# Performance work log

Hardware: AMD Instinct MI355X
Metric: run time of the kernel (lower is better)

## Reference

```python
import jax, jax.numpy as jnp
import numpy as np

N_QUBITS = 12
ENTANGLER_REPS = 2  # qml.layer(BasicEntanglerLayers, reps=2): 2 rings of CNOTs


def _apply_rx(state, theta, q, n):
    # state: (B, 2^n) complex; theta: (B,) per-sample RX angle on wire q
    B = state.shape[0]
    st = state.reshape(B, 2 ** q, 2, -1)
    c = jnp.cos(theta * 0.5)[:, None, None]
    s = jnp.sin(theta * 0.5)[:, None, None]
    s0, s1 = st[:, :, 0, :], st[:, :, 1, :]
    new0 = c * s0 - 1j * s * s1
    new1 = -1j * s * s0 + c * s1
    return jnp.stack([new0, new1], axis=2).reshape(B, -1)


def _apply_cnot(state, c, t, n):
    # CNOT with control wire c, target wire t (wire 0 = most significant bit)
    B = state.shape[0]
    st = state.reshape((B,) + (2,) * n)
    a0 = jnp.take(st, jnp.array([0]), axis=c + 1)
    a1 = jnp.take(st, jnp.array([1]), axis=c + 1)
    a1 = jnp.flip(a1, axis=t + 1)  # flip target when control = 1
    return jnp.concatenate([a0, a1], axis=c + 1).reshape(B, -1)


def quantum_latent(z, q_params):
    # Batched statevector simulation of: RX(z_i + p_i) on each wire,
    # then ENTANGLER_REPS rings of CNOT(i, (i+1)%n), measure <Z_i> per wire.
    B, n = z.shape
    theta = z + q_params[None, :]
    state = jnp.zeros((B, 2 ** n), dtype=jnp.complex64).at[:, 0].set(1.0)
    for q in range(n):
        state = _apply_rx(state, theta[:, q], q, n)
    for _ in range(ENTANGLER_REPS):
        for q in range(n):
            state = _apply_cnot(state, q, (q + 1) % n, n)
    probs = jnp.real(state * jnp.conj(state))  # (B, 2^n)
    expz = []
    for q in range(n):
        p = probs.reshape(B, 2 ** q, 2, -1)
        expz.append(p[:, :, 0, :].sum(axis=(1, 2)) - p[:, :, 1, :].sum(axis=(1, 2)))
    return jnp.stack(expz, axis=1)  # (B, n) float32


def setup_inputs() -> dict:
    key = jax.random.key(0)
    ks = jax.random.split(key, 16)
    B, D, H1, H2, L = 2048, 4096, 2048, 1024, N_QUBITS

    def lin(k, i, o):
        return (jax.random.normal(k, (o, i), jnp.float32) / np.sqrt(i)).astype(jnp.float32)

    return {
        "x": jax.random.normal(ks[0], (B, D), jnp.float32),
        "enc_w1": lin(ks[1], D, H1), "enc_b1": jnp.zeros((H1,), jnp.float32),
        "enc_w2": lin(ks[2], H1, H2), "enc_b2": jnp.zeros((H2,), jnp.float32),
        "enc_w3": lin(ks[3], H2, L), "enc_b3": jnp.zeros((L,), jnp.float32),
        "q_params": 0.1 * jax.random.normal(ks[4], (L,), jnp.float32),
        "dec_w1": lin(ks[5], L, H2), "dec_b1": jnp.zeros((H2,), jnp.float32),
        "dec_w2": lin(ks[6], H2, H1), "dec_b2": jnp.zeros((H1,), jnp.float32),
        "dec_w3": lin(ks[7], H1, D), "dec_b3": jnp.zeros((D,), jnp.float32),
    }


def reference(x, enc_w1, enc_b1, enc_w2, enc_b2, enc_w3, enc_b3, q_params,
              dec_w1, dec_b1, dec_w2, dec_b2, dec_w3, dec_b3):
    # encoder: Linear+ReLU (dropout=0 -> identity), Linear+ReLU, Linear
    h = jax.nn.relu(x @ enc_w1.T + enc_b1)
    h = jax.nn.relu(h @ enc_w2.T + enc_b2)
    z = h @ enc_w3.T + enc_b3  # (B, latent_dim)
    qz = quantum_latent(z, q_params)  # (B, latent_dim)
    # decoder (reversed hidden dims)
    h = jax.nn.relu(qz @ dec_w1.T + dec_b1)
    h = jax.nn.relu(h @ dec_w2.T + dec_b2)
    recon = h @ dec_w3.T + dec_b3  # (B, input_dim)
    return recon
```

## Files before the change

kernel.cpp:

```cpp
#include <hip/hip_runtime.h>
#include <hip/hip_bf16.h>


typedef __bf16 bf16x8 __attribute__((ext_vector_type(8)));
typedef __bf16 bf16x4 __attribute__((ext_vector_type(4)));
typedef float  f32x4  __attribute__((ext_vector_type(4)));

__device__ __forceinline__ void async16(const void* g, void* l) {
    __builtin_amdgcn_global_load_lds(
        (const __attribute__((address_space(1))) unsigned int*)g,
        (__attribute__((address_space(3))) unsigned int*)l,
        16, 0, 0);
}

template<int VM> __device__ __forceinline__ void wait_vm_lgkm0() {
    if constexpr (VM == 0)      asm volatile("s_waitcnt vmcnt(0) lgkmcnt(0)" ::: "memory");
    else if constexpr (VM == 4) asm volatile("s_waitcnt vmcnt(4) lgkmcnt(0)" ::: "memory");
    else if constexpr (VM == 6) asm volatile("s_waitcnt vmcnt(6) lgkmcnt(0)" ::: "memory");
    else if constexpr (VM == 8) asm volatile("s_waitcnt vmcnt(8) lgkmcnt(0)" ::: "memory");
    else static_assert(VM == 0 || VM == 4 || VM == 6 || VM == 8, "unsupported VM");
}

template <int BM, int BN, typename TOUT, bool RELU>
__global__ __launch_bounds__(256) void gemm_pipe(
    const __bf16* __restrict__ A, const __bf16* __restrict__ W,
    const float* __restrict__ bias, TOUT* __restrict__ C,
    int M, int N, int K)
{
    constexpr int CHA = BM / 32, CHB = BN / 32, LLOADS = CHA + CHB;
    constexpr int ABYTES = BM * 128, BUFB = (BM + BN) * 128;
    constexpr int WMR = BM / 2, WNC = BN / 2;
    constexpr int NI = WMR / 16, NJ = WNC / 16;

    extern __shared__ char smem[];

    const int t    = threadIdx.x;
    const int lane = t & 63;
    const int w    = t >> 6;
    const int bm   = blockIdx.y * BM;
    const int bn   = blockIdx.x * BN;

    const int sr  = lane >> 3;
    const int scs = (lane & 7) ^ sr;
    const __bf16* gA = A + (size_t)(bm + w * 8 + sr) * K + scs * 8;
    const __bf16* gB = W + (size_t)(bn + w * 8 + sr) * K + scs * 8;

    const int lm = lane & 15;
    const int lh = lane >> 4;
    const int wm = w >> 1, wn = w & 1;
    const int axor = lm & 7;

    f32x4 acc[NI][NJ] = {};

    auto STAGE = [&](int buf, int tt) {
        char* la = smem + buf * BUFB + w * 1024;
        char* lb = smem + buf * BUFB + ABYTES + w * 1024;
        const __bf16* ga = gA + (size_t)tt * 64;
        const __bf16* gb = gB + (size_t)tt * 64;
        #pragma unroll
        for (int j = 0; j < CHA; ++j) async16(ga + (size_t)32 * K * j, la + j * 4096);
        #pragma unroll
        for (int j = 0; j < CHB; ++j) async16(gb + (size_t)32 * K * j, lb + j * 4096);
    };

    auto COMPUTE = [&](int buf) {
        char* base = smem + buf * BUFB;
        bf16x8 a[2][NI], b[2][NJ];
        #pragma unroll
        for (int kh = 0; kh < 2; ++kh) {
            #pragma unroll
            for (int i = 0; i < NI; ++i)
                a[kh][i] = *(const bf16x8*)(base + (wm * WMR + i * 16 + lm) * 128
                                            + ((kh * 4 + lh) ^ axor) * 16);
            #pragma unroll
            for (int j = 0; j < NJ; ++j)
                b[kh][j] = *(const bf16x8*)(base + ABYTES + (wn * WNC + j * 16 + lm) * 128
                                            + ((kh * 4 + lh) ^ axor) * 16);
        }
        __builtin_amdgcn_s_setprio(1);
        #pragma unroll
        for (int kh = 0; kh < 2; ++kh)
            #pragma unroll
            for (int i = 0; i < NI; ++i)
                #pragma unroll
                for (int j = 0; j < NJ; ++j)
                    acc[i][j] = __builtin_amdgcn_mfma_f32_16x16x32_bf16(
                        a[kh][i], b[kh][j], acc[i][j], 0, 0, 0);
        __builtin_amdgcn_s_setprio(0);
    };

    const int NT = K >> 6;
    STAGE(0, 0);
    STAGE(1, 1);

    for (int tt = 0; tt < NT; ++tt) {
        if (tt < NT - 1) wait_vm_lgkm0<LLOADS>();
        else             wait_vm_lgkm0<0>();
        __builtin_amdgcn_s_barrier();
        __builtin_amdgcn_sched_barrier(0);
        COMPUTE(tt & 1);
        if (tt + 2 < NT) {
            asm volatile("s_waitcnt lgkmcnt(0)" ::: "memory");
            __builtin_amdgcn_s_barrier();
            __builtin_amdgcn_sched_barrier(0);
            STAGE(tt & 1, tt + 2);
        }
    }

    #pragma unroll
    for (int i = 0; i < NI; ++i) {
        const int row0 = bm + wm * WMR + i * 16 + lh * 4;
        #pragma unroll
        for (int j = 0; j < NJ; ++j) {
            const int col = bn + wn * WNC + j * 16 + lm;
            const float bv = bias[col];
            #pragma unroll
            for (int r = 0; r < 4; ++r) {
                float v = acc[i][j][r] + bv;
                if (RELU) v = fmaxf(v, 0.f);
                C[(size_t)(row0 + r) * N + col] = (TOUT)v;
            }
        }
    }
}

__device__ __forceinline__ void cvt8(const float* __restrict__ src,
                                     __bf16* __restrict__ dst, int g) {
    const float4* p = reinterpret_cast<const float4*>(src) + (size_t)g * 2;
    float4 a = p[0], b = p[1];
    bf16x8 v;
    v[0] = (__bf16)a.x; v[1] = (__bf16)a.y; v[2] = (__bf16)a.z; v[3] = (__bf16)a.w;
    v[4] = (__bf16)b.x; v[5] = (__bf16)b.y; v[6] = (__bf16)b.z; v[7] = (__bf16)b.w;
    reinterpret_cast<bf16x8*>(dst)[g] = v;
}

__global__ __launch_bounds__(256) void cvt_pair(
    const float* __restrict__ s0, __bf16* __restrict__ d0, int n0,
    const float* __restrict__ s1, __bf16* __restrict__ d1)
{
    int i = blockIdx.x * 256 + threadIdx.x;
    if (i < n0) cvt8(s0, d0, i);
    else        cvt8(s1, d1, i - n0);
}

__global__ __launch_bounds__(256) void cvt_triple(
    const float* __restrict__ s0, __bf16* __restrict__ d0, int n0,
    const float* __restrict__ s1, __bf16* __restrict__ d1, int n1,
    const float* __restrict__ s2, __bf16* __restrict__ d2)
{
    int i = blockIdx.x * 256 + threadIdx.x;
    if (i < n0)           cvt8(s0, d0, i);
    else if (i < n0 + n1) cvt8(s1, d1, i - n0);
    else                  cvt8(s2, d2, i - n0 - n1);
}

__constant__ unsigned short kSMask[12] = {
    0xAAB, 0xFFD, 0xFFA, 0xFF5, 0xFEA, 0xFD5,
    0xFAA, 0xF55, 0xEAA, 0xD55, 0xAAA, 0x555
};

__global__ __launch_bounds__(256) void enc3q_dec1(
    const float* __restrict__ H2,
    const float* __restrict__ W3,
    const float* __restrict__ b3,
    const float* __restrict__ qp,
    const float* __restrict__ dW1,
    const float* __restrict__ db1,
    __bf16* __restrict__ H3)
{
    const int b    = blockIdx.x;
    const int t    = threadIdx.x;
    const int lane = t & 63;
    const int wid  = t >> 6;

    float h[4];
    #pragma unroll
    for (int i = 0; i < 4; ++i) h[i] = H2[(size_t)b * 1024 + t + i * 256];

    __shared__ float wred[4][12];
    __shared__ float ctheta[12];
    __shared__ float qz[12];

    #pragma unroll 1
    for (int n = 0; n < 12; ++n) {
        float p = 0.f;
        #pragma unroll
        for (int i = 0; i < 4; ++i)
            p = fmaf(h[i], W3[n * 1024 + t + i * 256], p);
        #pragma unroll
        for (int off = 32; off > 0; off >>= 1)
            p += __shfl_down(p, off);
        if (lane == 0) wred[wid][n] = p;
    }
    __syncthreads();

    if (t < 12) {
        float z = wred[0][t] + wred[1][t] + wred[2][t] + wred[3][t]
                + b3[t] + qp[t];
        ctheta[t] = cosf(z);
    }
    __syncthreads();

    if (t < 12) {
        const unsigned m = kSMask[t];
        float prod = 1.f;
        #pragma unroll
        for (int j = 0; j < 12; ++j)
            if ((m >> j) & 1) prod *= ctheta[j];
        qz[t] = prod;
    }
    __syncthreads();

    bf16x4 v;
    #pragma unroll
    for (int j = 0; j < 4; ++j) {
        const int n = t * 4 + j;
        float acc = db1[n];
        #pragma unroll
        for (int k = 0; k < 12; ++k)
            acc = fmaf(qz[k], dW1[n * 12 + k], acc);
        v[j] = (__bf16)fmaxf(acc, 0.f);
    }
    *reinterpret_cast<bf16x4*>(&H3[(size_t)b * 1024 + t * 4]) = v;
}

extern "C" void kernel_launch(void* const* d_in, const int* in_sizes, int n_in,
                              void* d_out, int out_size, void* d_ws, size_t ws_size,
                              hipStream_t stream) {
    const float* x   = (const float*)d_in[0];
    const float* w1  = (const float*)d_in[1];
    const float* b1  = (const float*)d_in[2];
    const float* w2  = (const float*)d_in[3];
    const float* b2  = (const float*)d_in[4];
    const float* w3  = (const float*)d_in[5];
    const float* b3  = (const float*)d_in[6];
    const float* qp  = (const float*)d_in[7];
    const float* dw1 = (const float*)d_in[8];
    const float* db1 = (const float*)d_in[9];
    const float* dw2 = (const float*)d_in[10];
    const float* db2 = (const float*)d_in[11];
    const float* dw3 = (const float*)d_in[12];
    const float* db3 = (const float*)d_in[13];
    float* out = (float*)d_out;

    const int B = 2048, D = 4096, H1 = 2048, H2 = 1024;

    char* ws = (char*)d_ws;
    __bf16* xb   = (__bf16*)(ws);
    __bf16* dw3b = (__bf16*)(ws);
    __bf16* w1b  = (__bf16*)(ws + 16777216);
    float*  h2f  = (float*) (ws + 16777216);
    __bf16* w2b  = (__bf16*)(ws + 25165824);
    __bf16* h3b  = (__bf16*)(ws + 25165824);
    __bf16* dw2b = (__bf16*)(ws + 29360128);
    __bf16* h1b  = (__bf16*)(ws + 33554432);
    __bf16* h4b  = (__bf16*)(ws + 33554432);

    dim3 blk(256);

    cvt_pair<<<dim3(8192), blk, 0, stream>>>(x, xb, 1048576, w1, w1b);

    gemm_pipe<128, 64, __bf16, true><<<dim3(H1 / 64, B / 128), blk, 49152, stream>>>(
        xb, w1b, b1, h1b, B, H1, D);

    cvt_triple<<<dim3(6144), blk, 0, stream>>>(w2, w2b, 262144,
                                               dw2, dw2b, 262144,
                                               dw3, dw3b);

    gemm_pipe<64, 64, float, true><<<dim3(H2 / 64, B / 64), blk, 32768, stream>>>(
        h1b, w2b, b2, h2f, B, H2, H1);

    enc3q_dec1<<<dim3(B), blk, 0, stream>>>(h2f, w3, b3, qp, dw1, db1, h3b);

    gemm_pipe<128, 64, __bf16, true><<<dim3(H1 / 64, B / 128), blk, 49152, stream>>>(
        h3b, dw2b, db2, h4b, B, H1, H2);

    gemm_pipe<128, 128, float, false><<<dim3(D / 128, B / 128), blk, 65536, stream>>>(
        h4b, dw3b, db3, out, B, D, H1);
}
```

Measured before the change: 153.8 us.

## Load GEMM B operand directly into registers with triple-buffered LDS A tiles

Rewrites the GEMM kernel so the weight (B) operand is loaded straight from global memory into registers, double-buffered across k-steps, and no longer staged through LDS. Only the A tile goes through LDS, now in a three-buffer rotation with a single barrier per k-step. It also adds an XCD-style block-index swizzle and switches all four GEMMs to larger tiles, sized to 256 blocks. This is meant to cut LDS traffic and barriers, but it raises register pressure, brings uncoalesced direct global loads of B, and leaves fewer blocks per launch.

```diff
diff --git a/kernel.cpp b/kernel.cpp
--- a/kernel.cpp
+++ b/kernel.cpp
@@ -16,96 +16,117 @@
 template<int VM> __device__ __forceinline__ void wait_vm_lgkm0() {
     if constexpr (VM == 0)      asm volatile("s_waitcnt vmcnt(0) lgkmcnt(0)" ::: "memory");
     else if constexpr (VM == 4) asm volatile("s_waitcnt vmcnt(4) lgkmcnt(0)" ::: "memory");
-    else if constexpr (VM == 6) asm volatile("s_waitcnt vmcnt(6) lgkmcnt(0)" ::: "memory");
     else if constexpr (VM == 8) asm volatile("s_waitcnt vmcnt(8) lgkmcnt(0)" ::: "memory");
-    else static_assert(VM == 0 || VM == 4 || VM == 6 || VM == 8, "unsupported VM");
+    else static_assert(VM == 0 || VM == 4 || VM == 8, "unsupported VM");
 }
 
 template <int BM, int BN, typename TOUT, bool RELU>
-__global__ __launch_bounds__(256) void gemm_pipe(
+__global__ __launch_bounds__(256) void gemm_bdir(
     const __bf16* __restrict__ A, const __bf16* __restrict__ W,
     const float* __restrict__ bias, TOUT* __restrict__ C,
     int M, int N, int K)
 {
-    constexpr int CHA = BM / 32, CHB = BN / 32, LLOADS = CHA + CHB;
-    constexpr int ABYTES = BM * 128, BUFB = (BM + BN) * 128;
+    constexpr int CHA = BM / 32;
     constexpr int WMR = BM / 2, WNC = BN / 2;
     constexpr int NI = WMR / 16, NJ = WNC / 16;
+    constexpr int ABYTES = BM * 128;
 
     extern __shared__ char smem[];
 
-    const int t    = threadIdx.x;
-    const int lane = t & 63;
-    const int w    = t >> 6;
-    const int bm   = blockIdx.y * BM;
-    const int bn   = blockIdx.x * BN;
+    const int t = threadIdx.x, lane = t & 63, w = t >> 6;
+
+    const int gx = gridDim.x, gy = gridDim.y;
+    const int lin = blockIdx.y * gx + blockIdx.x;
+    const int cpx = (gx * gy) >> 3;
+    const int swz = (lin & 7) * cpx + (lin >> 3);
+    const int bm = (swz % gy) * BM;
+    const int bn = (swz / gy) * BN;
 
     const int sr  = lane >> 3;
     const int scs = (lane & 7) ^ sr;
     const __bf16* gA = A + (size_t)(bm + w * 8 + sr) * K + scs * 8;
-    const __bf16* gB = W + (size_t)(bn + w * 8 + sr) * K + scs * 8;
-
-    const int lm = lane & 15;
-    const int lh = lane >> 4;
+
+    const int lm = lane & 15, lh = lane >> 4;
     const int wm = w >> 1, wn = w & 1;
     const int axor = lm & 7;
 
+    const __bf16* gB = W + (size_t)(bn + wn * WNC + lm) * K + lh * 8;
+
     f32x4 acc[NI][NJ] = {};
-
-    auto STAGE = [&](int buf, int tt) {
-        char* la = smem + buf * BUFB + w * 1024;
-        char* lb = smem + buf * BUFB + ABYTES + w * 1024;
+    bf16x8 bP[2][NJ], bQ[2][NJ];
+
+    auto STAGE = [&](char* dst, int tt) {
         const __bf16* ga = gA + (size_t)tt * 64;
+        #pragma unroll
+        for (int j = 0; j < CHA; ++j)
+            async16(ga + (size_t)32 * K * j, dst + w * 1024 + j * 4096);
+    };
+    auto LOADB = [&](bf16x8 (&dst)[2][NJ], int tt) {
         const __bf16* gb = gB + (size_t)tt * 64;
         #pragma unroll
-        for (int j = 0; j < CHA; ++j) async16(ga + (size_t)32 * K * j, la + j * 4096);
-        #pragma unroll
-        for (int j = 0; j < CHB; ++j) async16(gb + (size_t)32 * K * j, lb + j * 4096);
+        for (int kh = 0; kh < 2; ++kh)
+            #pragma unroll
+            for (int j = 0; j < NJ; ++j)
+                dst[kh][j] = *(const bf16x8*)(gb + (size_t)j * 16 * K + kh * 32);
     };
-
-    auto COMPUTE = [&](int buf) {
-        char* base = smem + buf * BUFB;
-        bf16x8 a[2][NI], b[2][NJ];
+    auto COMPUTE = [&](const char* base, bf16x8 (&bf)[2][NJ]) {
         #pragma unroll
         for (int kh = 0; kh < 2; ++kh) {
+            bf16x8 a[NI];
             #pragma unroll
             for (int i = 0; i < NI; ++i)
-                a[kh][i] = *(const bf16x8*)(base + (wm * WMR + i * 16 + lm) * 128
-                                            + ((kh * 4 + lh) ^ axor) * 16);
-            #pragma unroll
-            for (int j = 0; j < NJ; ++j)
-                b[kh][j] = *(const bf16x8*)(base + ABYTES + (wn * WNC + j * 16 + lm) * 128
-                                            + ((kh * 4 + lh) ^ axor) * 16);
-        }
-        __builtin_amdgcn_s_setprio(1);
-        #pragma unroll
-        for (int kh = 0; kh < 2; ++kh)
+                a[i] = *(const bf16x8*)(base + (wm * WMR + i * 16 + lm) * 128
+                                        + ((kh * 4 + lh) ^ axor) * 16);
+            __builtin_amdgcn_s_setprio(1);
             #pragma unroll
             for (int i = 0; i < NI; ++i)
                 #pragma unroll
                 for (int j = 0; j < NJ; ++j)
                     acc[i][j] = __builtin_amdgcn_mfma_f32_16x16x32_bf16(
-                        a[kh][i], b[kh][j], acc[i][j], 0, 0, 0);
-        __builtin_amdgcn_s_setprio(0);
+                        a[i], bf[kh][j], acc[i][j], 0, 0, 0);
+            __builtin_amdgcn_s_setprio(0);
+        }
     };
 
+    char* a0 = smem;
+    char* a1 = smem + ABYTES;
+    char* a2 = smem + 2 * ABYTES;
+
     const int NT = K >> 6;
-    STAGE(0, 0);
-    STAGE(1, 1);
-
-    for (int tt = 0; tt < NT; ++tt) {
-        if (tt < NT - 1) wait_vm_lgkm0<LLOADS>();
-        else             wait_vm_lgkm0<0>();
+    STAGE(a0, 0);
+    LOADB(bP, 0);
+    STAGE(a1, 1);
+
+    for (int tt = 0; tt < NT - 2; tt += 2) {
+        wait_vm_lgkm0<CHA>();
         __builtin_amdgcn_s_barrier();
         __builtin_amdgcn_sched_barrier(0);
-        COMPUTE(tt & 1);
-        if (tt + 2 < NT) {
-            asm volatile("s_waitcnt lgkmcnt(0)" ::: "memory");
-            __builtin_amdgcn_s_barrier();
-            __builtin_amdgcn_sched_barrier(0);
-            STAGE(tt & 1, tt + 2);
-        }
-    }
+        LOADB(bQ, tt + 1);
+        STAGE(a2, tt + 2);
+        __builtin_amdgcn_sched_barrier(0);
+        COMPUTE(a0, bP);
+
+        wait_vm_lgkm0<CHA>();
+        __builtin_amdgcn_s_barrier();
+        __builtin_amdgcn_sched_barrier(0);
+        if (tt + 2 < NT - 2 || true) {}
+        LOADB(bP, tt + 2);
+        if (tt + 3 < NT) STAGE(a0, tt + 3);
+        __builtin_amdgcn_sched_barrier(0);
+        COMPUTE(a1, bQ);
+
+        char* tmp = a0; a0 = a2; a2 = a1; a1 = tmp;
+    }
+    wait_vm_lgkm0<CHA>();
+    __builtin_amdgcn_s_barrier();
+    __builtin_amdgcn_sched_barrier(0);
+    LOADB(bQ, NT - 1);
+    __builtin_amdgcn_sched_barrier(0);
+    COMPUTE(a0, bP);
+    wait_vm_lgkm0<0>();
+    __builtin_amdgcn_s_barrier();
+    __builtin_amdgcn_sched_barrier(0);
+    COMPUTE(a1, bQ);
 
     #pragma unroll
     for (int i = 0; i < NI; ++i) {
@@ -245,6 +266,19 @@
 
     const int B = 2048, D = 4096, H1 = 2048, H2 = 1024;
 
+    static int attr_done = 0;
+    if (!attr_done) {
+        hipFuncSetAttribute((const void*)&gemm_bdir<128, 128, __bf16, true>,
+                            hipFuncAttributeMaxDynamicSharedMemorySize, 49152);
+        hipFuncSetAttribute((const void*)&gemm_bdir<128, 64, float, true>,
+                            hipFuncAttributeMaxDynamicSharedMemorySize, 49152);
+        hipFuncSetAttribute((const void*)&gemm_bdir<256, 64, __bf16, true>,
+                            hipFuncAttributeMaxDynamicSharedMemorySize, 98304);
+        hipFuncSetAttribute((const void*)&gemm_bdir<256, 128, float, false>,
+                            hipFuncAttributeMaxDynamicSharedMemorySize, 98304);
+        attr_done = 1;
+    }
+
     char* ws = (char*)d_ws;
     __bf16* xb   = (__bf16*)(ws);
     __bf16* dw3b = (__bf16*)(ws);
@@ -260,21 +294,21 @@
 
     cvt_pair<<<dim3(8192), blk, 0, stream>>>(x, xb, 1048576, w1, w1b);
 
-    gemm_pipe<128, 64, __bf16, true><<<dim3(H1 / 64, B / 128), blk, 49152, stream>>>(
+    gemm_bdir<128, 128, __bf16, true><<<dim3(16, 16), blk, 49152, stream>>>(
         xb, w1b, b1, h1b, B, H1, D);
 
     cvt_triple<<<dim3(6144), blk, 0, stream>>>(w2, w2b, 262144,
                                                dw2, dw2b, 262144,
                                                dw3, dw3b);
 
-    gemm_pipe<64, 64, float, true><<<dim3(H2 / 64, B / 64), blk, 32768, stream>>>(
+    gemm_bdir<128, 64, float, true><<<dim3(16, 16), blk, 49152, stream>>>(
         h1b, w2b, b2, h2f, B, H2, H1);
 
     enc3q_dec1<<<dim3(B), blk, 0, stream>>>(h2f, w3, b3, qp, dw1, db1, h3b);
 
-    gemm_pipe<128, 64, __bf16, true><<<dim3(H1 / 64, B / 128), blk, 49152, stream>>>(
+    gemm_bdir<256, 64, __bf16, true><<<dim3(32, 8), blk, 98304, stream>>>(
         h3b, dw2b, db2, h4b, B, H1, H2);
 
-    gemm_pipe<128, 128, float, false><<<dim3(D / 128, B / 128), blk, 65536, stream>>>(
+    gemm_bdir<256, 128, float, false><<<dim3(32, 8), blk, 98304, stream>>>(
         h4b, dw3b, db3, out, B, D, H1);
 }
```

After: 256.3 us. +66.7%, slower.

## Switch GEMMs to triple-buffered ring pipeline with larger tiles and grid swizzle

Applied to the files above, without the earlier changes.

Replaces the double-buffered GEMM with a three-buffer LDS ring, so the next stage's async loads are issued before computing the current tile and one barrier per iteration is dropped. Tile sizes are enlarged for all four GEMMs to 128x128, 128x64 and 128x256, all on a 16x16 grid. Block indices are remapped through an XCD-style swizzle to improve L2 locality. LDS use per block rises, up to 144KB, which lowers occupancy, and the kernel now relies on setting the max dynamic shared memory attribute.

```diff
diff --git a/kernel.cpp b/kernel.cpp
--- a/kernel.cpp
+++ b/kernel.cpp
@@ -13,98 +13,97 @@
         16, 0, 0);
 }
 
-template<int VM> __device__ __forceinline__ void wait_vm_lgkm0() {
-    if constexpr (VM == 0)      asm volatile("s_waitcnt vmcnt(0) lgkmcnt(0)" ::: "memory");
-    else if constexpr (VM == 4) asm volatile("s_waitcnt vmcnt(4) lgkmcnt(0)" ::: "memory");
-    else if constexpr (VM == 6) asm volatile("s_waitcnt vmcnt(6) lgkmcnt(0)" ::: "memory");
-    else if constexpr (VM == 8) asm volatile("s_waitcnt vmcnt(8) lgkmcnt(0)" ::: "memory");
-    else static_assert(VM == 0 || VM == 4 || VM == 6 || VM == 8, "unsupported VM");
+template<int VM> __device__ __forceinline__ void wait_vm() {
+    if constexpr (VM == 0)       asm volatile("s_waitcnt vmcnt(0) lgkmcnt(0)" ::: "memory");
+    else if constexpr (VM == 6)  asm volatile("s_waitcnt vmcnt(6) lgkmcnt(0)" ::: "memory");
+    else if constexpr (VM == 8)  asm volatile("s_waitcnt vmcnt(8) lgkmcnt(0)" ::: "memory");
+    else if constexpr (VM == 12) asm volatile("s_waitcnt vmcnt(12) lgkmcnt(0)" ::: "memory");
+    else static_assert(VM == 0 || VM == 6 || VM == 8 || VM == 12, "unsupported VM");
 }
 
 template <int BM, int BN, typename TOUT, bool RELU>
-__global__ __launch_bounds__(256) void gemm_pipe(
+__global__ __launch_bounds__(256) void gemm_ring(
     const __bf16* __restrict__ A, const __bf16* __restrict__ W,
     const float* __restrict__ bias, TOUT* __restrict__ C,
     int M, int N, int K)
 {
-    constexpr int CHA = BM / 32, CHB = BN / 32, LLOADS = CHA + CHB;
+    constexpr int CHA = BM / 32, CHB = BN / 32, L = CHA + CHB;
     constexpr int ABYTES = BM * 128, BUFB = (BM + BN) * 128;
     constexpr int WMR = BM / 2, WNC = BN / 2;
     constexpr int NI = WMR / 16, NJ = WNC / 16;
 
     extern __shared__ char smem[];
 
-    const int t    = threadIdx.x;
-    const int lane = t & 63;
-    const int w    = t >> 6;
-    const int bm   = blockIdx.y * BM;
-    const int bn   = blockIdx.x * BN;
+    const int t = threadIdx.x, lane = t & 63, w = t >> 6;
+
+    const int gx = gridDim.x, gy = gridDim.y;
+    const int lin = blockIdx.y * gx + blockIdx.x;
+    const int cpx = (gx * gy) >> 3;
+    const int swz = (lin & 7) * cpx + (lin >> 3);
+    const int bm = (swz % gy) * BM;
+    const int bn = (swz / gy) * BN;
 
     const int sr  = lane >> 3;
     const int scs = (lane & 7) ^ sr;
     const __bf16* gA = A + (size_t)(bm + w * 8 + sr) * K + scs * 8;
     const __bf16* gB = W + (size_t)(bn + w * 8 + sr) * K + scs * 8;
 
-    const int lm = lane & 15;
-    const int lh = lane >> 4;
+    const int lm = lane & 15, lh = lane >> 4;
     const int wm = w >> 1, wn = w & 1;
     const int axor = lm & 7;
 
     f32x4 acc[NI][NJ] = {};
 
-    auto STAGE = [&](int buf, int tt) {
-        char* la = smem + buf * BUFB + w * 1024;
-        char* lb = smem + buf * BUFB + ABYTES + w * 1024;
+    auto STAGE = [&](char* buf, int tt) {
         const __bf16* ga = gA + (size_t)tt * 64;
         const __bf16* gb = gB + (size_t)tt * 64;
+        char* la = buf + w * 1024;
+        char* lb = buf + ABYTES + w * 1024;
         #pragma unroll
         for (int j = 0; j < CHA; ++j) async16(ga + (size_t)32 * K * j, la + j * 4096);
         #pragma unroll
         for (int j = 0; j < CHB; ++j) async16(gb + (size_t)32 * K * j, lb + j * 4096);
     };
 
-    auto COMPUTE = [&](int buf) {
-        char* base = smem + buf * BUFB;
-        bf16x8 a[2][NI], b[2][NJ];
+    auto COMPUTE = [&](const char* base) {
         #pragma unroll
         for (int kh = 0; kh < 2; ++kh) {
+            const int sl = ((kh * 4 + lh) ^ axor) * 16;
+            bf16x8 a[NI], b[NJ];
             #pragma unroll
             for (int i = 0; i < NI; ++i)
-                a[kh][i] = *(const bf16x8*)(base + (wm * WMR + i * 16 + lm) * 128
-                                            + ((kh * 4 + lh) ^ axor) * 16);
+                a[i] = *(const bf16x8*)(base + (wm * WMR + i * 16 + lm) * 128 + sl);
             #pragma unroll
             for (int j = 0; j < NJ; ++j)
-                b[kh][j] = *(const bf16x8*)(base + ABYTES + (wn * WNC + j * 16 + lm) * 128
-                                            + ((kh * 4 + lh) ^ axor) * 16);
-        }
-        __builtin_amdgcn_s_setprio(1);
-        #pragma unroll
-        for (int kh = 0; kh < 2; ++kh)
+                b[j] = *(const bf16x8*)(base + ABYTES + (wn * WNC + j * 16 + lm) * 128 + sl);
+            __builtin_amdgcn_s_setprio(1);
             #pragma unroll
             for (int i = 0; i < NI; ++i)
                 #pragma unroll
                 for (int j = 0; j < NJ; ++j)
                     acc[i][j] = __builtin_amdgcn_mfma_f32_16x16x32_bf16(
-                        a[kh][i], b[kh][j], acc[i][j], 0, 0, 0);
-        __builtin_amdgcn_s_setprio(0);
+                        a[i], b[j], acc[i][j], 0, 0, 0);
+            __builtin_amdgcn_s_setprio(0);
+        }
     };
 
     const int NT = K >> 6;
-    STAGE(0, 0);
-    STAGE(1, 1);
+    char* cur = smem;
+    char* nxt = smem + BUFB;
+    char* fre = smem + 2 * BUFB;
+
+    STAGE(cur, 0);
+    STAGE(nxt, 1);
 
     for (int tt = 0; tt < NT; ++tt) {
-        if (tt < NT - 1) wait_vm_lgkm0<LLOADS>();
-        else             wait_vm_lgkm0<0>();
+        if (tt < NT - 1) wait_vm<L>();
+        else             wait_vm<0>();
         __builtin_amdgcn_s_barrier();
         __builtin_amdgcn_sched_barrier(0);
-        COMPUTE(tt & 1);
-        if (tt + 2 < NT) {
-            asm volatile("s_waitcnt lgkmcnt(0)" ::: "memory");
-            __builtin_amdgcn_s_barrier();
-            __builtin_amdgcn_sched_barrier(0);
-            STAGE(tt & 1, tt + 2);
-        }
+        if (tt + 2 < NT) STAGE(fre, tt + 2);
+        __builtin_amdgcn_sched_barrier(0);
+        COMPUTE(cur);
+        char* tmp = cur; cur = nxt; nxt = fre; fre = tmp;
     }
 
     #pragma unroll
@@ -245,6 +244,17 @@
 
     const int B = 2048, D = 4096, H1 = 2048, H2 = 1024;
 
+    static int attr_done = 0;
+    if (!attr_done) {
+        hipFuncSetAttribute((const void*)&gemm_ring<128, 128, __bf16, true>,
+                            hipFuncAttributeMaxDynamicSharedMemorySize, 98304);
+        hipFuncSetAttribute((const void*)&gemm_ring<128, 64, float, true>,
+                            hipFuncAttributeMaxDynamicSharedMemorySize, 73728);
+        hipFuncSetAttribute((const void*)&gemm_ring<128, 256, float, false>,
+                            hipFuncAttributeMaxDynamicSharedMemorySize, 147456);
+        attr_done = 1;
+    }
+
     char* ws = (char*)d_ws;
     __bf16* xb   = (__bf16*)(ws);
     __bf16* dw3b = (__bf16*)(ws);
@@ -257,24 +267,25 @@
     __bf16* h4b  = (__bf16*)(ws + 33554432);
 
     dim3 blk(256);
+    dim3 grid16(16, 16);
 
     cvt_pair<<<dim3(8192), blk, 0, stream>>>(x, xb, 1048576, w1, w1b);
 
-    gemm_pipe<128, 64, __bf16, true><<<dim3(H1 / 64, B / 128), blk, 49152, stream>>>(
+    gemm_ring<128, 128, __bf16, true><<<grid16, blk, 98304, stream>>>(
         xb, w1b, b1, h1b, B, H1, D);
 
     cvt_triple<<<dim3(6144), blk, 0, stream>>>(w2, w2b, 262144,
                                                dw2, dw2b, 262144,
                                                dw3, dw3b);
 
-    gemm_pipe<64, 64, float, true><<<dim3(H2 / 64, B / 64), blk, 32768, stream>>>(
+    gemm_ring<128, 64, float, true><<<grid16, blk, 73728, stream>>>(
         h1b, w2b, b2, h2f, B, H2, H1);
 
     enc3q_dec1<<<dim3(B), blk, 0, stream>>>(h2f, w3, b3, qp, dw1, db1, h3b);
 
-    gemm_pipe<128, 64, __bf16, true><<<dim3(H1 / 64, B / 128), blk, 49152, stream>>>(
+    gemm_ring<128, 128, __bf16, true><<<grid16, blk, 98304, stream>>>(
         h3b, dw2b, db2, h4b, B, H1, H2);
 
-    gemm_pipe<128, 128, float, false><<<dim3(D / 128, B / 128), blk, 65536, stream>>>(
+    gemm_ring<128, 256, float, false><<<grid16, blk, 147456, stream>>>(
         h4b, dw3b, db3, out, B, D, H1);
 }
```

Result: slower. 166.5 us (+8.3%).

## Fuse weight conversion into first GEMM tail blocks and swizzle tile order

Applied to the files above, without the earlier changes.

Makes the first GEMM launch 256 extra blocks that convert the remaining fp32 weights (w2, dw2, dw3) to bf16 alongside the matmul, removing the separate cvt_triple launch when the workspace is large enough. All GEMMs switch to a 1D grid with an XCD-style block swizzle for cache locality. The compute loop now interleaves LDS loads and MFMAs per k-half to cut register pressure. The cost is a larger workspace layout, an added branch, and one-time function attribute setup.

```diff
diff --git a/kernel.cpp b/kernel.cpp
--- a/kernel.cpp
+++ b/kernel.cpp
@@ -13,7 +13,7 @@
         16, 0, 0);
 }
 
-template<int VM> __device__ __forceinline__ void wait_vm_lgkm0() {
+template<int VM> __device__ __forceinline__ void wait_vm() {
     if constexpr (VM == 0)      asm volatile("s_waitcnt vmcnt(0) lgkmcnt(0)" ::: "memory");
     else if constexpr (VM == 4) asm volatile("s_waitcnt vmcnt(4) lgkmcnt(0)" ::: "memory");
     else if constexpr (VM == 6) asm volatile("s_waitcnt vmcnt(6) lgkmcnt(0)" ::: "memory");
@@ -21,32 +21,58 @@
     else static_assert(VM == 0 || VM == 4 || VM == 6 || VM == 8, "unsupported VM");
 }
 
-template <int BM, int BN, typename TOUT, bool RELU>
+__device__ __forceinline__ void cvt8(const float* __restrict__ src,
+                                     __bf16* __restrict__ dst, int g) {
+    const float4* p = reinterpret_cast<const float4*>(src) + (size_t)g * 2;
+    float4 a = p[0], b = p[1];
+    bf16x8 v;
+    v[0] = (__bf16)a.x; v[1] = (__bf16)a.y; v[2] = (__bf16)a.z; v[3] = (__bf16)a.w;
+    v[4] = (__bf16)b.x; v[5] = (__bf16)b.y; v[6] = (__bf16)b.z; v[7] = (__bf16)b.w;
+    reinterpret_cast<bf16x8*>(dst)[g] = v;
+}
+
+template <int BM, int BN, int GX, int GY, typename TOUT, bool RELU, bool TAIL>
 __global__ __launch_bounds__(256) void gemm_pipe(
     const __bf16* __restrict__ A, const __bf16* __restrict__ W,
     const float* __restrict__ bias, TOUT* __restrict__ C,
-    int M, int N, int K)
+    int M, int N, int K,
+    const float* __restrict__ cs0, __bf16* __restrict__ cd0, int cn0,
+    const float* __restrict__ cs1, __bf16* __restrict__ cd1, int cn1,
+    const float* __restrict__ cs2, __bf16* __restrict__ cd2, int cn2)
 {
-    constexpr int CHA = BM / 32, CHB = BN / 32, LLOADS = CHA + CHB;
+    constexpr int CHA = BM / 32, CHB = BN / 32, L = CHA + CHB;
     constexpr int ABYTES = BM * 128, BUFB = (BM + BN) * 128;
     constexpr int WMR = BM / 2, WNC = BN / 2;
     constexpr int NI = WMR / 16, NJ = WNC / 16;
 
     extern __shared__ char smem[];
 
-    const int t    = threadIdx.x;
-    const int lane = t & 63;
-    const int w    = t >> 6;
-    const int bm   = blockIdx.y * BM;
-    const int bn   = blockIdx.x * BN;
+    const int lin = blockIdx.x;
+
+    if (TAIL && lin >= GX * GY) {
+        const int total = cn0 + cn1 + cn2;
+        const int nthr  = 256 * 256;
+        for (int g = (lin - GX * GY) * 256 + threadIdx.x; g < total; g += nthr) {
+            if (g < cn0)            cvt8(cs0, cd0, g);
+            else if (g < cn0 + cn1) cvt8(cs1, cd1, g - cn0);
+            else                    cvt8(cs2, cd2, g - cn0 - cn1);
+        }
+        return;
+    }
+
+    const int t = threadIdx.x, lane = t & 63, w = t >> 6;
+
+    constexpr int CPX = (GX * GY) >> 3;
+    const int swz = (lin & 7) * CPX + (lin >> 3);
+    const int bm = (swz % GY) * BM;
+    const int bn = (swz / GY) * BN;
 
     const int sr  = lane >> 3;
     const int scs = (lane & 7) ^ sr;
     const __bf16* gA = A + (size_t)(bm + w * 8 + sr) * K + scs * 8;
     const __bf16* gB = W + (size_t)(bn + w * 8 + sr) * K + scs * 8;
 
-    const int lm = lane & 15;
-    const int lh = lane >> 4;
+    const int lm = lane & 15, lh = lane >> 4;
     const int wm = w >> 1, wn = w & 1;
     const int axor = lm & 7;
 
@@ -64,29 +90,26 @@
     };
 
     auto COMPUTE = [&](int buf) {
-        char* base = smem + buf * BUFB;
-        bf16x8 a[2][NI], b[2][NJ];
+        const char* base = smem + buf * BUFB;
         #pragma unroll
         for (int kh = 0; kh < 2; ++kh) {
+            const int sl = ((kh * 4 + lh) ^ axor) * 16;
+            bf16x8 a[NI], b[NJ];
             #pragma unroll
             for (int i = 0; i < NI; ++i)
-                a[kh][i] = *(const bf16x8*)(base + (wm * WMR + i * 16 + lm) * 128
-                                            + ((kh * 4 + lh) ^ axor) * 16);
+                a[i] = *(const bf16x8*)(base + (wm * WMR + i * 16 + lm) * 128 + sl);
             #pragma unroll
             for (int j = 0; j < NJ; ++j)
-                b[kh][j] = *(const bf16x8*)(base + ABYTES + (wn * WNC + j * 16 + lm) * 128
-                                            + ((kh * 4 + lh) ^ axor) * 16);
-        }
-        __builtin_amdgcn_s_setprio(1);
-        #pragma unroll
-        for (int kh = 0; kh < 2; ++kh)
+                b[j] = *(const bf16x8*)(base + ABYTES + (wn * WNC + j * 16 + lm) * 128 + sl);
+            __builtin_amdgcn_s_setprio(1);
             #pragma unroll
             for (int i = 0; i < NI; ++i)
                 #pragma unroll
                 for (int j = 0; j < NJ; ++j)
                     acc[i][j] = __builtin_amdgcn_mfma_f32_16x16x32_bf16(
-                        a[kh][i], b[kh][j], acc[i][j], 0, 0, 0);
-        __builtin_amdgcn_s_setprio(0);
+                        a[i], b[j], acc[i][j], 0, 0, 0);
+            __builtin_amdgcn_s_setprio(0);
+        }
     };
 
     const int NT = K >> 6;
@@ -94,8 +117,8 @@
     STAGE(1, 1);
 
     for (int tt = 0; tt < NT; ++tt) {
-        if (tt < NT - 1) wait_vm_lgkm0<LLOADS>();
-        else             wait_vm_lgkm0<0>();
+        if (tt < NT - 1) wait_vm<L>();
+        else             wait_vm<0>();
         __builtin_amdgcn_s_barrier();
         __builtin_amdgcn_sched_barrier(0);
         COMPUTE(tt & 1);
@@ -122,16 +145,6 @@
             }
         }
     }
-}
-
-__device__ __forceinline__ void cvt8(const float* __restrict__ src,
-                                     __bf16* __restrict__ dst, int g) {
-    const float4* p = reinterpret_cast<const float4*>(src) + (size_t)g * 2;
-    float4 a = p[0], b = p[1];
-    bf16x8 v;
-    v[0] = (__bf16)a.x; v[1] = (__bf16)a.y; v[2] = (__bf16)a.z; v[3] = (__bf16)a.w;
-    v[4] = (__bf16)b.x; v[5] = (__bf16)b.y; v[6] = (__bf16)b.z; v[7] = (__bf16)b.w;
-    reinterpret_cast<bf16x8*>(dst)[g] = v;
 }
 
 __global__ __launch_bounds__(256) void cvt_pair(
@@ -245,36 +258,85 @@
 
     const int B = 2048, D = 4096, H1 = 2048, H2 = 1024;
 
+    static int attr_done = 0;
+    if (!attr_done) {
+        hipFuncSetAttribute((const void*)&gemm_pipe<128, 64, 32, 16, __bf16, true, true>,
+                            hipFuncAttributeMaxDynamicSharedMemorySize, 49152);
+        hipFuncSetAttribute((const void*)&gemm_pipe<128, 64, 32, 16, __bf16, true, false>,
+                            hipFuncAttributeMaxDynamicSharedMemorySize, 49152);
+        hipFuncSetAttribute((const void*)&gemm_pipe<64, 64, 16, 32, float, true, false>,
+                            hipFuncAttributeMaxDynamicSharedMemorySize, 32768);
+        hipFuncSetAttribute((const void*)&gemm_pipe<128, 128, 32, 16, float, false, false>,
+                            hipFuncAttributeMaxDynamicSharedMemorySize, 65536);
+        attr_done = 1;
+    }
+
+    dim3 blk(256);
     char* ws = (char*)d_ws;
-    __bf16* xb   = (__bf16*)(ws);
-    __bf16* dw3b = (__bf16*)(ws);
-    __bf16* w1b  = (__bf16*)(ws + 16777216);
-    float*  h2f  = (float*) (ws + 16777216);
-    __bf16* w2b  = (__bf16*)(ws + 25165824);
-    __bf16* h3b  = (__bf16*)(ws + 25165824);
-    __bf16* dw2b = (__bf16*)(ws + 29360128);
-    __bf16* h1b  = (__bf16*)(ws + 33554432);
-    __bf16* h4b  = (__bf16*)(ws + 33554432);
-
-    dim3 blk(256);
-
-    cvt_pair<<<dim3(8192), blk, 0, stream>>>(x, xb, 1048576, w1, w1b);
-
-    gemm_pipe<128, 64, __bf16, true><<<dim3(H1 / 64, B / 128), blk, 49152, stream>>>(
-        xb, w1b, b1, h1b, B, H1, D);
-
-    cvt_triple<<<dim3(6144), blk, 0, stream>>>(w2, w2b, 262144,
-                                               dw2, dw2b, 262144,
-                                               dw3, dw3b);
-
-    gemm_pipe<64, 64, float, true><<<dim3(H2 / 64, B / 64), blk, 32768, stream>>>(
-        h1b, w2b, b2, h2f, B, H2, H1);
-
-    enc3q_dec1<<<dim3(B), blk, 0, stream>>>(h2f, w3, b3, qp, dw1, db1, h3b);
-
-    gemm_pipe<128, 64, __bf16, true><<<dim3(H1 / 64, B / 128), blk, 49152, stream>>>(
-        h3b, dw2b, db2, h4b, B, H1, H2);
-
-    gemm_pipe<128, 128, float, false><<<dim3(D / 128, B / 128), blk, 65536, stream>>>(
-        h4b, dw3b, db3, out, B, D, H1);
-}
+
+    if (ws_size >= (size_t)67108864) {
+        __bf16* xb   = (__bf16*)(ws);
+        __bf16* w1b  = (__bf16*)(ws + 16777216);
+        __bf16* h1b  = (__bf16*)(ws + 33554432);
+        __bf16* w2b  = (__bf16*)(ws + 41943040);
+        __bf16* dw2b = (__bf16*)(ws + 46137344);
+        __bf16* dw3b = (__bf16*)(ws + 50331648);
+        float*  h2f  = (float*) (ws);
+        __bf16* h3b  = (__bf16*)(ws + 8388608);
+        __bf16* h4b  = (__bf16*)(ws + 16777216);
+
+        cvt_pair<<<dim3(8192), blk, 0, stream>>>(x, xb, 1048576, w1, w1b);
+
+        gemm_pipe<128, 64, 32, 16, __bf16, true, true><<<dim3(768), blk, 49152, stream>>>(
+            xb, w1b, b1, h1b, B, H1, D,
+            w2, w2b, 262144, dw2, dw2b, 262144, dw3, dw3b, 1048576);
+
+        gemm_pipe<64, 64, 16, 32, float, true, false><<<dim3(512), blk, 32768, stream>>>(
+            h1b, w2b, b2, h2f, B, H2, H1,
+            nullptr, nullptr, 0, nullptr, nullptr, 0, nullptr, nullptr, 0);
+
+        enc3q_dec1<<<dim3(B), blk, 0, stream>>>(h2f, w3, b3, qp, dw1, db1, h3b);
+
+        gemm_pipe<128, 64, 32, 16, __bf16, true, false><<<dim3(512), blk, 49152, stream>>>(
+            h3b, dw2b, db2, h4b, B, H1, H2,
+            nullptr, nullptr, 0, nullptr, nullptr, 0, nullptr, nullptr, 0);
+
+        gemm_pipe<128, 128, 32, 16, float, false, false><<<dim3(512), blk, 65536, stream>>>(
+            h4b, dw3b, db3, out, B, D, H1,
+            nullptr, nullptr, 0, nullptr, nullptr, 0, nullptr, nullptr, 0);
+    } else {
+        __bf16* xb   = (__bf16*)(ws);
+        __bf16* dw3b = (__bf16*)(ws);
+        __bf16* w1b  = (__bf16*)(ws + 16777216);
+        float*  h2f  = (float*) (ws + 16777216);
+        __bf16* w2b  = (__bf16*)(ws + 25165824);
+        __bf16* h3b  = (__bf16*)(ws + 25165824);
+        __bf16* dw2b = (__bf16*)(ws + 29360128);
+        __bf16* h1b  = (__bf16*)(ws + 33554432);
+        __bf16* h4b  = (__bf16*)(ws + 33554432);
+
+        cvt_pair<<<dim3(8192), blk, 0, stream>>>(x, xb, 1048576, w1, w1b);
+
+        gemm_pipe<128, 64, 32, 16, __bf16, true, false><<<dim3(512), blk, 49152, stream>>>(
+            xb, w1b, b1, h1b, B, H1, D,
+            nullptr, nullptr, 0, nullptr, nullptr, 0, nullptr, nullptr, 0);
+
+        cvt_triple<<<dim3(6144), blk, 0, stream>>>(w2, w2b, 262144,
+                                                   dw2, dw2b, 262144,
+                                                   dw3, dw3b);
+
+        gemm_pipe<64, 64, 16, 32, float, true, false><<<dim3(512), blk, 32768, stream>>>(
+            h1b, w2b, b2, h2f, B, H2, H1,
+            nullptr, nullptr, 0, nullptr, nullptr, 0, nullptr, nullptr, 0);
+
+        enc3q_dec1<<<dim3(B), blk, 0, stream>>>(h2f, w3, b3, qp, dw1, db1, h3b);
+
+        gemm_pipe<128, 64, 32, 16, __bf16, true, false><<<dim3(512), blk, 49152, stream>>>(
+            h3b, dw2b, db2, h4b, B, H1, H2,
+            nullptr, nullptr, 0, nullptr, nullptr, 0, nullptr, nullptr, 0);
+
+        gemm_pipe<128, 128, 32, 16, float, false, false><<<dim3(512), blk, 65536, stream>>>(
+            h4b, dw3b, db3, out, B, D, H1,
+            nullptr, nullptr, 0, nullptr, nullptr, 0, nullptr, nullptr, 0);
+    }
+}
```

After: 156.5 us. No clear change (+1.8%).
